# Performance work log

Measured on AMD Instinct MI355X. Metric: run time of the kernel, lower is better.

The kernel has to match this reference:

```python
import jax, jax.numpy as jnp
import numpy as np

B, T, C = 2, 2048, 1024
H, D = 16, 64


def setup_inputs() -> dict:
    key = jax.random.key(0)
    ks = jax.random.split(key, 6)
    s = 0.02
    return {
        "x": jax.random.normal(ks[0], (B, T, C), dtype=jnp.float32),
        "W_qkv": jax.random.normal(ks[1], (3 * H * D, C), dtype=jnp.float32) * s,
        "b_qkv": jnp.zeros((3 * H * D,), dtype=jnp.float32),
        "W_proj": jax.random.normal(ks[2], (C, H * D), dtype=jnp.float32) * s,
        "b_proj": jnp.zeros((C,), dtype=jnp.float32),
        "sink_logit": jnp.zeros((H,), dtype=jnp.float32),
    }


def reference(x, W_qkv, b_qkv, W_proj, b_proj, sink_logit):
    Bx, Tx, Cx = x.shape
    qkv = x @ W_qkv.T + b_qkv  # (B,T,3*H*D)
    q, k, v = jnp.split(qkv, 3, axis=-1)
    # (B,T,H,D) -> (B,H,T,D)
    q = q.reshape(Bx, Tx, H, D).transpose(0, 2, 1, 3)
    k = k.reshape(Bx, Tx, H, D).transpose(0, 2, 1, 3)
    v = v.reshape(Bx, Tx, H, D).transpose(0, 2, 1, 3)
    scale = 1.0 / jnp.sqrt(jnp.asarray(D, dtype=x.dtype))
    scores = jnp.einsum("bhqd,bhkd->bhqk", q, k) * scale  # (B,H,T,T)
    neg_inf = jnp.finfo(x.dtype).min
    causal = jnp.tril(jnp.ones((Tx, Tx), dtype=bool))
    scores = jnp.where(causal[None, None], scores, neg_inf)
    # sink slot: k_sink = 0 so its logit is just the learnable sink bias
    sink = jnp.broadcast_to(sink_logit[None, :, None, None], (Bx, H, Tx, 1))
    logits = jnp.concatenate([sink.astype(scores.dtype), scores], axis=-1)  # (B,H,T,T+1)
    probs = jax.nn.softmax(logits, axis=-1)
    # v_sink is zero, so drop sink column in the value contraction
    out = jnp.einsum("bhqk,bhkd->bhqd", probs[..., 1:], v)
    y = out.transpose(0, 2, 1, 3).reshape(Bx, Tx, H * D)
    return y @ W_proj.T + b_proj
```

## Files before the change

kernel.cpp:

```cpp
#include <hip/hip_runtime.h>
#include <hip/hip_bf16.h>

#define Bb 2
#define Tt 2048
#define Cc 1024
#define Hh 16
#define Dd 64

typedef __bf16 bf8 __attribute__((ext_vector_type(8)));
typedef __bf16 bf4 __attribute__((ext_vector_type(4)));
typedef float f4 __attribute__((ext_vector_type(4)));

typedef __attribute__((address_space(3))) void lds_void;
typedef const __attribute__((address_space(1))) void g_void;

__device__ __forceinline__ void gload_lds16(const __bf16* g, __bf16* l) {
  __builtin_amdgcn_global_load_lds((g_void*)g, (lds_void*)l, 16, 0, 0);
}

__device__ __forceinline__ float ex2(float x) { return __builtin_amdgcn_exp2f(x); }

__global__ __launch_bounds__(256) void cvt3_kernel(
    const float* __restrict__ a, __bf16* __restrict__ oa, int na,
    const float* __restrict__ b, __bf16* __restrict__ ob, int nb,
    const float* __restrict__ c, __bf16* __restrict__ oc) {
  int gi = blockIdx.x * 256 + threadIdx.x;
  const int t0 = na >> 3, t1 = t0 + (nb >> 3);
  const float* src; __bf16* dst; int idx;
  if (gi < t0)      { src = a; dst = oa; idx = gi; }
  else if (gi < t1) { src = b; dst = ob; idx = gi - t0; }
  else              { src = c; dst = oc; idx = gi - t1; }
  const float* p = src + (size_t)idx * 8;
  float4 u = *(const float4*)p;
  float4 v = *(const float4*)(p + 4);
  bf8 r;
  r[0] = (__bf16)u.x; r[1] = (__bf16)u.y; r[2] = (__bf16)u.z; r[3] = (__bf16)u.w;
  r[4] = (__bf16)v.x; r[5] = (__bf16)v.y; r[6] = (__bf16)v.z; r[7] = (__bf16)v.w;
  *(bf8*)(dst + (size_t)idx * 8) = r;
}

__global__ __launch_bounds__(256) void gemm128_kernel(
    const __bf16* __restrict__ A, const __bf16* __restrict__ W,
    const float* __restrict__ bias, int K,
    __bf16* __restrict__ q_ws, __bf16* __restrict__ k_ws,
    __bf16* __restrict__ v_ws)
{
  const int tid = threadIdx.x;
  const int lane = tid & 63, wave = tid >> 6;
  const int lr = lane & 15, lq = lane >> 4;
  const int m_blk = blockIdx.y * 128, n_blk = blockIdx.x * 128;
  const int wm = (wave & 1) * 64, wn = (wave >> 1) * 64;

  __shared__ __align__(16) __bf16 As[128 * 32];
  __shared__ __align__(16) __bf16 Bs[128 * 32];
  __shared__ __align__(16) __bf16 Epi[4][64 * 72];

  const int srow = tid >> 2, scol = (tid & 3) * 8;
  const __bf16* ag0 = A + (size_t)(m_blk + srow) * K + scol;
  const __bf16* ag1 = A + (size_t)(m_blk + 64 + srow) * K + scol;
  const __bf16* bg0 = W + (size_t)(n_blk + srow) * K + scol;
  const __bf16* bg1 = W + (size_t)(n_blk + 64 + srow) * K + scol;
  __bf16* al0 = As + tid * 8;
  __bf16* al1 = As + 2048 + tid * 8;
  __bf16* bl0 = Bs + tid * 8;
  __bf16* bl1 = Bs + 2048 + tid * 8;

  f4 acc[4][4] = {};
  for (int k0 = 0; k0 < K; k0 += 32) {
    gload_lds16(ag0 + k0, al0);
    gload_lds16(ag1 + k0, al1);
    gload_lds16(bg0 + k0, bl0);
    gload_lds16(bg1 + k0, bl1);
    __syncthreads();

    bf8 af[4], bfr[4];
    #pragma unroll
    for (int i = 0; i < 4; ++i)
      af[i] = *(const bf8*)&As[(wm + i * 16 + lr) * 32 + lq * 8];
    #pragma unroll
    for (int j = 0; j < 4; ++j)
      bfr[j] = *(const bf8*)&Bs[(wn + j * 16 + lr) * 32 + lq * 8];
    #pragma unroll
    for (int i = 0; i < 4; ++i)
      #pragma unroll
      for (int j = 0; j < 4; ++j)
        acc[i][j] = __builtin_amdgcn_mfma_f32_16x16x32_bf16(af[i], bfr[j], acc[i][j], 0, 0, 0);
    __syncthreads();
  }

  const int col0 = n_blk + wn;
  const int which = col0 >> 10;
  const int b = m_blk >> 11;
  const int h = (col0 & 1023) >> 6;
  const size_t bh = (size_t)b * Hh + h;

  if (which == 2) {
    __bf16* E = Epi[wave];
    #pragma unroll
    for (int j = 0; j < 4; ++j) {
      float bv = bias[col0 + j * 16 + lr];
      #pragma unroll
      for (int i = 0; i < 4; ++i)
        #pragma unroll
        for (int r = 0; r < 4; ++r)
          E[(j * 16 + lr) * 72 + i * 16 + lq * 4 + r] = (__bf16)(acc[i][j][r] + bv);
    }
    asm volatile("s_waitcnt lgkmcnt(0)" ::: "memory");
    const int t0 = (m_blk + wm) & 2047;
    const int dd = lane >> 3, tl = (lane & 7) * 8;
    #pragma unroll
    for (int di = 0; di < 8; ++di) {
      int d = di * 8 + dd;
      bf8 vv = *(const bf8*)&E[d * 72 + tl];
      *(bf8*)&v_ws[(bh * Dd + d) * Tt + t0 + tl] = vv;
    }
  } else {
    __bf16* dst = (which == 0) ? q_ws : k_ws;
    const float scl = (which == 0) ? 0.18033688011112042f : 1.0f;
    #pragma unroll
    for (int i = 0; i < 4; ++i) {
      #pragma unroll
      for (int j = 0; j < 4; ++j) {
        #pragma unroll
        for (int r = 0; r < 4; ++r) {
          int row = m_blk + wm + i * 16 + lq * 4 + r;
          int col = col0 + j * 16 + lr;
          float val = (acc[i][j][r] + bias[col]) * scl;
          int d = col & 63, t = row & 2047;
          dst[(bh * Tt + t) * Dd + d] = (__bf16)val;
        }
      }
    }
  }
}

__global__ __launch_bounds__(256) void gemm64_kernel(
    const __bf16* __restrict__ A, const __bf16* __restrict__ W,
    const float* __restrict__ bias, int K, float* __restrict__ out, int ldo)
{
  const int tid = threadIdx.x;
  const int lane = tid & 63, wave = tid >> 6;
  const int lr = lane & 15, lq = lane >> 4;
  const int m_blk = blockIdx.y * 64, n_blk = blockIdx.x * 64;
  const int wm = (wave & 1) * 32, wn = (wave >> 1) * 32;

  __shared__ __align__(16) __bf16 As[64 * 32];
  __shared__ __align__(16) __bf16 Bs[64 * 32];

  const int srow = tid >> 2, scol = (tid & 3) * 8;
  const __bf16* ag = A + (size_t)(m_blk + srow) * K + scol;
  const __bf16* bg = W + (size_t)(n_blk + srow) * K + scol;
  __bf16* al = As + tid * 8;
  __bf16* bl = Bs + tid * 8;

  f4 acc[2][2] = {};
  for (int k0 = 0; k0 < K; k0 += 32) {
    gload_lds16(ag + k0, al);
    gload_lds16(bg + k0, bl);
    __syncthreads();

    bf8 af[2], bfr[2];
    #pragma unroll
    for (int i = 0; i < 2; ++i)
      af[i] = *(const bf8*)&As[(wm + i * 16 + lr) * 32 + lq * 8];
    #pragma unroll
    for (int j = 0; j < 2; ++j)
      bfr[j] = *(const bf8*)&Bs[(wn + j * 16 + lr) * 32 + lq * 8];
    #pragma unroll
    for (int i = 0; i < 2; ++i)
      #pragma unroll
      for (int j = 0; j < 2; ++j)
        acc[i][j] = __builtin_amdgcn_mfma_f32_16x16x32_bf16(af[i], bfr[j], acc[i][j], 0, 0, 0);
    __syncthreads();
  }

  #pragma unroll
  for (int i = 0; i < 2; ++i)
    #pragma unroll
    for (int j = 0; j < 2; ++j)
      #pragma unroll
      for (int r = 0; r < 4; ++r) {
        int row = m_blk + wm + i * 16 + lq * 4 + r;
        int col = n_blk + wn + j * 16 + lr;
        out[(size_t)row * ldo + col] = acc[i][j][r] + bias[col];
      }
}

__global__ __launch_bounds__(512) void attn_kernel(
    const __bf16* __restrict__ q_ws, const __bf16* __restrict__ k_ws,
    const __bf16* __restrict__ v_ws, const float* __restrict__ sink,
    __bf16* __restrict__ y_ws)
{
  int bi = blockIdx.x;
  int qt, bhi;
  if (bi < 256) { qt = 15 - (bi >> 5); bhi = bi & 31; }
  else          { qt = (bi - 256) >> 5; bhi = (bi - 256) & 31; }
  const int h = bhi & (Hh - 1);
  const int b = bhi >> 4;
  const int tid = threadIdx.x;
  const int lane = tid & 63, wave = tid >> 6;
  const int lr = lane & 15, lq = lane >> 4;

  __shared__ __align__(16) __bf16 KsU[3][64 * 64];
  __shared__ __align__(16) __bf16 VtU[3][64 * 64];
  __shared__ __align__(16) __bf16 PsU[8][16 * 64];

  const __bf16* qp = q_ws + (size_t)bhi * Tt * Dd;
  const __bf16* kp = k_ws + (size_t)bhi * Tt * Dd;
  const __bf16* vp = v_ws + (size_t)bhi * Dd * Tt;

  const int qbase = qt * 128;
  const int qlo = qbase + wave * 16;

  bf8 qf[2];
  {
    const __bf16* qrow = qp + (size_t)(qlo + lr) * Dd;
    qf[0] = *(const bf8*)(qrow + lq * 8);
    qf[1] = *(const bf8*)(qrow + 32 + lq * 8);
  }

  float rs = 0.f;
  f4 o_acc[4] = {};

  const int srow_g = tid >> 3;
  const int sslot = tid & 7;
  const int nkt = 2 * qt + 2;

  auto stage = [&](int kt2, int bsel) {
    const int kbase2 = kt2 * 64;
    const int cc = sslot ^ (srow_g & 7);
    gload_lds16(kp + (size_t)(kbase2 + srow_g) * Dd + cc * 8,
                &KsU[bsel][wave * 512 + lane * 8]);
    gload_lds16(vp + (size_t)srow_g * Tt + kbase2 + cc * 8,
                &VtU[bsel][wave * 512 + lane * 8]);
  };

  auto computeS = [&](const __bf16* Kb, f4 (&sA)[4]) {
    #pragma unroll
    for (int nt = 0; nt < 4; ++nt) {
      const int krow = nt * 16 + lr;
      const int x7 = krow & 7;
      bf8 kb0 = *(const bf8*)&Kb[krow * 64 + ((lq ^ x7) * 8)];
      bf8 kb1 = *(const bf8*)&Kb[krow * 64 + (((4 + lq) ^ x7) * 8)];
      f4 c = {};
      c = __builtin_amdgcn_mfma_f32_16x16x32_bf16(kb0, qf[0], c, 0, 0, 0);
      c = __builtin_amdgcn_mfma_f32_16x16x32_bf16(kb1, qf[1], c, 0, 0, 0);
      sA[nt] = c;
    }
  };

  f4 s_cur[4], s_next[4];

  stage(0, 0);
  __syncthreads();
  stage(1, 1);
  computeS(KsU[0], s_cur);

  for (int kt = 0; kt < nkt; ++kt) {
    __syncthreads();
    if (kt + 2 < nkt) stage(kt + 2, (kt + 2) % 3);

    if (kt + 1 < nkt && (kt + 1) * 64 <= qlo + 15)
      computeS(KsU[(kt + 1) % 3], s_next);

    const int kbase = kt * 64;
    if (kbase <= qlo + 15) {
      __bf16* Pw = PsU[wave];
      const bool diag = (kbase + 63 > qlo);
      if (diag) {
        #pragma unroll
        for (int nt = 0; nt < 4; ++nt) {
          const int qg = qlo + lr;
          const int kg = kbase + nt * 16 + lq * 4;
          bf4 pb;
          #pragma unroll
          for (int r = 0; r < 4; ++r) {
            float sv = (kg + r > qg) ? -1e30f : s_cur[nt][r];
            float p = ex2(sv);
            rs += p;
            pb[r] = (__bf16)p;
          }
          const int G = (nt * 2 + (lq >> 1)) ^ (lr & 7);
          *(bf4*)&Pw[lr * 64 + G * 8 + (lq & 1) * 4] = pb;
        }
      } else {
        #pragma unroll
        for (int nt = 0; nt < 4; ++nt) {
          bf4 pb;
          #pragma unroll
          for (int r = 0; r < 4; ++r) {
            float p = ex2(s_cur[nt][r]);
            rs += p;
            pb[r] = (__bf16)p;
          }
          const int G = (nt * 2 + (lq >> 1)) ^ (lr & 7);
          *(bf4*)&Pw[lr * 64 + G * 8 + (lq & 1) * 4] = pb;
        }
      }
      asm volatile("s_waitcnt lgkmcnt(0)" ::: "memory");

      const __bf16* Vb = VtU[kt % 3];
      #pragma unroll
      for (int ks = 0; ks < 2; ++ks) {
        const int pg = ((ks * 4 + lq) ^ (lr & 7)) * 8;
        bf8 pa = *(const bf8*)&Pw[lr * 64 + pg];
        #pragma unroll
        for (int dt = 0; dt < 4; ++dt) {
          const int vrow = dt * 16 + lr;
          bf8 vb = *(const bf8*)&Vb[vrow * 64 + (((ks * 4 + lq) ^ (vrow & 7)) * 8)];
          o_acc[dt] = __builtin_amdgcn_mfma_f32_16x16x32_bf16(pa, vb, o_acc[dt], 0, 0, 0);
        }
      }
    }

    #pragma unroll
    for (int nt = 0; nt < 4; ++nt)
      s_cur[nt] = s_next[nt];
  }

  rs += __shfl_xor(rs, 16, 64);
  rs += __shfl_xor(rs, 32, 64);
  const float snk = ex2(sink[h] * 1.44269504f);
  float inv = 1.0f / (rs + snk);
  float invr[4];
  #pragma unroll
  for (int r = 0; r < 4; ++r)
    invr[r] = __shfl(inv, lq * 4 + r, 64);

  #pragma unroll
  for (int dt = 0; dt < 4; ++dt)
    #pragma unroll
    for (int r = 0; r < 4; ++r) {
      int qrow = qlo + lq * 4 + r;
      y_ws[((size_t)b * Tt + qrow) * Cc + h * Dd + dt * 16 + lr] =
          (__bf16)(o_acc[dt][r] * invr[r]);
    }
}

extern "C" void kernel_launch(void* const* d_in, const int* in_sizes, int n_in,
                              void* d_out, int out_size, void* d_ws, size_t ws_size,
                              hipStream_t stream) {
  const float* x      = (const float*)d_in[0];
  const float* W_qkv  = (const float*)d_in[1];
  const float* b_qkv  = (const float*)d_in[2];
  const float* W_proj = (const float*)d_in[3];
  const float* b_proj = (const float*)d_in[4];
  const float* sinkp  = (const float*)d_in[5];
  float* out = (float*)d_out;

  const size_t n_x    = (size_t)Bb * Tt * Cc;
  const size_t n_wqkv = (size_t)3 * Hh * Dd * Cc;
  const size_t n_wprj = (size_t)Cc * Hh * Dd;
  const size_t nqkv   = (size_t)Bb * Hh * Tt * Dd;

  __bf16* xb     = (__bf16*)d_ws;
  __bf16* wqkvb  = xb + n_x;
  __bf16* wprojb = wqkvb + n_wqkv;
  __bf16* q_ws   = wprojb + n_wprj;
  __bf16* k_ws   = q_ws + nqkv;
  __bf16* v_ws   = k_ws + nqkv;
  __bf16* y_ws   = xb;

  dim3 blk(256);
  const int cvt_blocks = (int)((n_x + n_wqkv + n_wprj) / 8 / 256);
  cvt3_kernel<<<cvt_blocks, blk, 0, stream>>>(x, xb, (int)n_x,
                                              W_qkv, wqkvb, (int)n_wqkv,
                                              W_proj, wprojb);

  gemm128_kernel<<<dim3(3 * Cc / 128, Bb * Tt / 128), blk, 0, stream>>>(
      xb, wqkvb, b_qkv, Cc, q_ws, k_ws, v_ws);
  attn_kernel<<<dim3(512), dim3(512), 0, stream>>>(q_ws, k_ws, v_ws, sinkp, y_ws);
  gemm64_kernel<<<dim3(Cc / 64, Bb * Tt / 64), blk, 0, stream>>>(
      y_ws, wprojb, b_proj, Hh * Dd, out, Cc);
}
```

Measured before the change: 180.3 us.

## Double-buffer QKV GEMM loads and shrink attention tiles to 64 queries

The QKV GEMM now double-buffers its A/B tiles in shared memory, reusing the epilogue buffer. The next k-slice's global-to-LDS load is issued before computing the current one, and one barrier per iteration is dropped. The attention kernel moves from 128-query blocks of 8 waves to 64-query blocks of 4 waves, launched as 1024 blocks. It goes from triple to double buffering, drops the software-pipelined score prefetch and the per-wave causal skip, and aims at better occupancy and load balance at the cost of less intra-block overlap.

```diff
diff --git a/kernel.cpp b/kernel.cpp
--- a/kernel.cpp
+++ b/kernel.cpp
@@ -51,28 +51,35 @@
   const int m_blk = blockIdx.y * 128, n_blk = blockIdx.x * 128;
   const int wm = (wave & 1) * 64, wn = (wave >> 1) * 64;
 
-  __shared__ __align__(16) __bf16 As[128 * 32];
-  __shared__ __align__(16) __bf16 Bs[128 * 32];
-  __shared__ __align__(16) __bf16 Epi[4][64 * 72];
+  __shared__ __align__(16) __bf16 smem[4 * 64 * 72];
+  __bf16* AsB = smem;
+  __bf16* BsB = smem + 8192;
 
   const int srow = tid >> 2, scol = (tid & 3) * 8;
   const __bf16* ag0 = A + (size_t)(m_blk + srow) * K + scol;
   const __bf16* ag1 = A + (size_t)(m_blk + 64 + srow) * K + scol;
   const __bf16* bg0 = W + (size_t)(n_blk + srow) * K + scol;
   const __bf16* bg1 = W + (size_t)(n_blk + 64 + srow) * K + scol;
-  __bf16* al0 = As + tid * 8;
-  __bf16* al1 = As + 2048 + tid * 8;
-  __bf16* bl0 = Bs + tid * 8;
-  __bf16* bl1 = Bs + 2048 + tid * 8;
+
+  auto stage = [&](int k0, int bsel) {
+    __bf16* as = AsB + bsel * 4096;
+    __bf16* bs = BsB + bsel * 4096;
+    gload_lds16(ag0 + k0, as + tid * 8);
+    gload_lds16(ag1 + k0, as + 2048 + tid * 8);
+    gload_lds16(bg0 + k0, bs + tid * 8);
+    gload_lds16(bg1 + k0, bs + 2048 + tid * 8);
+  };
 
   f4 acc[4][4] = {};
-  for (int k0 = 0; k0 < K; k0 += 32) {
-    gload_lds16(ag0 + k0, al0);
-    gload_lds16(ag1 + k0, al1);
-    gload_lds16(bg0 + k0, bl0);
-    gload_lds16(bg1 + k0, bl1);
+  const int nk = K >> 5;
+
+  stage(0, 0);
+  for (int k = 0; k < nk; ++k) {
     __syncthreads();
-
+    if (k + 1 < nk) stage((k + 1) * 32, (k + 1) & 1);
+
+    const __bf16* As = AsB + (k & 1) * 4096;
+    const __bf16* Bs = BsB + (k & 1) * 4096;
     bf8 af[4], bfr[4];
     #pragma unroll
     for (int i = 0; i < 4; ++i)
@@ -85,8 +92,8 @@
       #pragma unroll
       for (int j = 0; j < 4; ++j)
         acc[i][j] = __builtin_amdgcn_mfma_f32_16x16x32_bf16(af[i], bfr[j], acc[i][j], 0, 0, 0);
-    __syncthreads();
-  }
+  }
+  __syncthreads();
 
   const int col0 = n_blk + wn;
   const int which = col0 >> 10;
@@ -95,7 +102,7 @@
   const size_t bh = (size_t)b * Hh + h;
 
   if (which == 2) {
-    __bf16* E = Epi[wave];
+    __bf16* E = smem + wave * 4608;
     #pragma unroll
     for (int j = 0; j < 4; ++j) {
       float bv = bias[col0 + j * 16 + lr];
@@ -186,30 +193,30 @@
       }
 }
 
-__global__ __launch_bounds__(512) void attn_kernel(
+__global__ __launch_bounds__(256) void attn_kernel(
     const __bf16* __restrict__ q_ws, const __bf16* __restrict__ k_ws,
     const __bf16* __restrict__ v_ws, const float* __restrict__ sink,
     __bf16* __restrict__ y_ws)
 {
   int bi = blockIdx.x;
   int qt, bhi;
-  if (bi < 256) { qt = 15 - (bi >> 5); bhi = bi & 31; }
-  else          { qt = (bi - 256) >> 5; bhi = (bi - 256) & 31; }
+  if (bi < 512) { qt = 31 - (bi >> 5); bhi = bi & 31; }
+  else          { qt = (bi - 512) >> 5; bhi = (bi - 512) & 31; }
   const int h = bhi & (Hh - 1);
   const int b = bhi >> 4;
   const int tid = threadIdx.x;
   const int lane = tid & 63, wave = tid >> 6;
   const int lr = lane & 15, lq = lane >> 4;
 
-  __shared__ __align__(16) __bf16 KsU[3][64 * 64];
-  __shared__ __align__(16) __bf16 VtU[3][64 * 64];
-  __shared__ __align__(16) __bf16 PsU[8][16 * 64];
+  __shared__ __align__(16) __bf16 KsU[2][64 * 64];
+  __shared__ __align__(16) __bf16 VtU[2][64 * 64];
+  __shared__ __align__(16) __bf16 PsU[4][16 * 64];
 
   const __bf16* qp = q_ws + (size_t)bhi * Tt * Dd;
   const __bf16* kp = k_ws + (size_t)bhi * Tt * Dd;
   const __bf16* vp = v_ws + (size_t)bhi * Dd * Tt;
 
-  const int qbase = qt * 128;
+  const int qbase = qt * 64;
   const int qlo = qbase + wave * 16;
 
   bf8 qf[2];
@@ -222,20 +229,33 @@
   float rs = 0.f;
   f4 o_acc[4] = {};
 
-  const int srow_g = tid >> 3;
+  const int srow_lo = tid >> 3;
   const int sslot = tid & 7;
-  const int nkt = 2 * qt + 2;
+  const int nkt = qt + 1;
 
   auto stage = [&](int kt2, int bsel) {
     const int kbase2 = kt2 * 64;
-    const int cc = sslot ^ (srow_g & 7);
-    gload_lds16(kp + (size_t)(kbase2 + srow_g) * Dd + cc * 8,
-                &KsU[bsel][wave * 512 + lane * 8]);
-    gload_lds16(vp + (size_t)srow_g * Tt + kbase2 + cc * 8,
-                &VtU[bsel][wave * 512 + lane * 8]);
+    #pragma unroll
+    for (int ii = 0; ii < 2; ++ii) {
+      const int r = ii * 32 + srow_lo;
+      const int cc = sslot ^ (r & 7);
+      gload_lds16(kp + (size_t)(kbase2 + r) * Dd + cc * 8,
+                  &KsU[bsel][ii * 2048 + tid * 8]);
+      gload_lds16(vp + (size_t)r * Tt + kbase2 + cc * 8,
+                  &VtU[bsel][ii * 2048 + tid * 8]);
+    }
   };
 
-  auto computeS = [&](const __bf16* Kb, f4 (&sA)[4]) {
+  stage(0, 0);
+  for (int kt = 0; kt < nkt; ++kt) {
+    __syncthreads();
+    if (kt + 1 < nkt) stage(kt + 1, (kt + 1) & 1);
+
+    const __bf16* Kb = KsU[kt & 1];
+    const __bf16* Vb = VtU[kt & 1];
+    const int kbase = kt * 64;
+
+    f4 s[4];
     #pragma unroll
     for (int nt = 0; nt < 4; ++nt) {
       const int krow = nt * 16 + lr;
@@ -245,77 +265,53 @@
       f4 c = {};
       c = __builtin_amdgcn_mfma_f32_16x16x32_bf16(kb0, qf[0], c, 0, 0, 0);
       c = __builtin_amdgcn_mfma_f32_16x16x32_bf16(kb1, qf[1], c, 0, 0, 0);
-      sA[nt] = c;
-    }
-  };
-
-  f4 s_cur[4], s_next[4];
-
-  stage(0, 0);
-  __syncthreads();
-  stage(1, 1);
-  computeS(KsU[0], s_cur);
-
-  for (int kt = 0; kt < nkt; ++kt) {
-    __syncthreads();
-    if (kt + 2 < nkt) stage(kt + 2, (kt + 2) % 3);
-
-    if (kt + 1 < nkt && (kt + 1) * 64 <= qlo + 15)
-      computeS(KsU[(kt + 1) % 3], s_next);
-
-    const int kbase = kt * 64;
-    if (kbase <= qlo + 15) {
-      __bf16* Pw = PsU[wave];
-      const bool diag = (kbase + 63 > qlo);
-      if (diag) {
+      s[nt] = c;
+    }
+
+    __bf16* Pw = PsU[wave];
+    if (kt == qt) {
+      #pragma unroll
+      for (int nt = 0; nt < 4; ++nt) {
+        const int qg = qlo + lr;
+        const int kg = kbase + nt * 16 + lq * 4;
+        bf4 pb;
         #pragma unroll
-        for (int nt = 0; nt < 4; ++nt) {
-          const int qg = qlo + lr;
-          const int kg = kbase + nt * 16 + lq * 4;
-          bf4 pb;
-          #pragma unroll
-          for (int r = 0; r < 4; ++r) {
-            float sv = (kg + r > qg) ? -1e30f : s_cur[nt][r];
-            float p = ex2(sv);
-            rs += p;
-            pb[r] = (__bf16)p;
-          }
-          const int G = (nt * 2 + (lq >> 1)) ^ (lr & 7);
-          *(bf4*)&Pw[lr * 64 + G * 8 + (lq & 1) * 4] = pb;
+        for (int r = 0; r < 4; ++r) {
+          float sv = (kg + r > qg) ? -1e30f : s[nt][r];
+          float p = ex2(sv);
+          rs += p;
+          pb[r] = (__bf16)p;
         }
-      } else {
+        const int G = (nt * 2 + (lq >> 1)) ^ (lr & 7);
+        *(bf4*)&Pw[lr * 64 + G * 8 + (lq & 1) * 4] = pb;
+      }
+    } else {
+      #pragma unroll
+      for (int nt = 0; nt < 4; ++nt) {
+        bf4 pb;
         #pragma unroll
-        for (int nt = 0; nt < 4; ++nt) {
-          bf4 pb;
-          #pragma unroll
-          for (int r = 0; r < 4; ++r) {
-            float p = ex2(s_cur[nt][r]);
-            rs += p;
-            pb[r] = (__bf16)p;
-          }
-          const int G = (nt * 2 + (lq >> 1)) ^ (lr & 7);
-          *(bf4*)&Pw[lr * 64 + G * 8 + (lq & 1) * 4] = pb;
+        for (int r = 0; r < 4; ++r) {
+          float p = ex2(s[nt][r]);
+          rs += p;
+          pb[r] = (__bf16)p;
         }
-      }
-      asm volatile("s_waitcnt lgkmcnt(0)" ::: "memory");
-
-      const __bf16* Vb = VtU[kt % 3];
-      #pragma unroll
-      for (int ks = 0; ks < 2; ++ks) {
-        const int pg = ((ks * 4 + lq) ^ (lr & 7)) * 8;
-        bf8 pa = *(const bf8*)&Pw[lr * 64 + pg];
-        #pragma unroll
-        for (int dt = 0; dt < 4; ++dt) {
-          const int vrow = dt * 16 + lr;
-          bf8 vb = *(const bf8*)&Vb[vrow * 64 + (((ks * 4 + lq) ^ (vrow & 7)) * 8)];
-          o_acc[dt] = __builtin_amdgcn_mfma_f32_16x16x32_bf16(pa, vb, o_acc[dt], 0, 0, 0);
-        }
-      }
-    }
-
-    #pragma unroll
-    for (int nt = 0; nt < 4; ++nt)
-      s_cur[nt] = s_next[nt];
+        const int G = (nt * 2 + (lq >> 1)) ^ (lr & 7);
+        *(bf4*)&Pw[lr * 64 + G * 8 + (lq & 1) * 4] = pb;
+      }
+    }
+    asm volatile("s_waitcnt lgkmcnt(0)" ::: "memory");
+
+    #pragma unroll
+    for (int ks = 0; ks < 2; ++ks) {
+      const int pg = ((ks * 4 + lq) ^ (lr & 7)) * 8;
+      bf8 pa = *(const bf8*)&Pw[lr * 64 + pg];
+      #pragma unroll
+      for (int dt = 0; dt < 4; ++dt) {
+        const int vrow = dt * 16 + lr;
+        bf8 vb = *(const bf8*)&Vb[vrow * 64 + (((ks * 4 + lq) ^ (vrow & 7)) * 8)];
+        o_acc[dt] = __builtin_amdgcn_mfma_f32_16x16x32_bf16(pa, vb, o_acc[dt], 0, 0, 0);
+      }
+    }
   }
 
   rs += __shfl_xor(rs, 16, 64);
@@ -369,7 +365,7 @@
 
   gemm128_kernel<<<dim3(3 * Cc / 128, Bb * Tt / 128), blk, 0, stream>>>(
       xb, wqkvb, b_qkv, Cc, q_ws, k_ws, v_ws);
-  attn_kernel<<<dim3(512), dim3(512), 0, stream>>>(q_ws, k_ws, v_ws, sinkp, y_ws);
+  attn_kernel<<<dim3(1024), blk, 0, stream>>>(q_ws, k_ws, v_ws, sinkp, y_ws);
   gemm64_kernel<<<dim3(Cc / 64, Bb * Tt / 64), blk, 0, stream>>>(
       y_ws, wprojb, b_proj, Hh * Dd, out, Cc);
 }
```

Result: faster. 171.6 us (-4.8%).
